# Performance work log

Hardware: AMD Instinct MI355X
Metric: run time of the kernel (lower is better)

Reference implementation:

```python
import jax, jax.numpy as jnp
import numpy as np

TOKENS_B, TOKENS_S, N_IN, N_OUT = 8, 2048, 4096, 4096
N8, N4 = 2048, 2048  # channels per format


def setup_inputs() -> dict:
    key = jax.random.key(0)
    k = jax.random.split(key, 7)
    x = jax.random.normal(k[0], (TOKENS_B, TOKENS_S, N_IN), dtype=jnp.float32)
    # int8-format group: values in [-128, 127], per-output-channel scale
    q8 = jax.random.randint(k[1], (N8, N_IN), -128, 128, dtype=jnp.int32)
    s8 = jax.random.uniform(k[2], (N8, 1), dtype=jnp.float32) * 0.01 + 1e-4
    # int4-format group: values in [-8, 7], per-output-channel scale
    q4 = jax.random.randint(k[3], (N4, N_IN), -8, 8, dtype=jnp.int32)
    s4 = jax.random.uniform(k[4], (N4, 1), dtype=jnp.float32) * 0.1 + 1e-4
    # inverse permutation restoring original channel order from [fmt8 | fmt4] concat
    inv_perm = jax.random.permutation(k[5], N_OUT).astype(jnp.int32)
    bias = jax.random.normal(k[6], (N_OUT,), dtype=jnp.float32) * 0.01
    return {"x": x, "q8": q8, "s8": s8, "q4": q4, "s4": s4,
            "inv_perm": inv_perm, "bias": bias}


def reference(x, q8, s8, q4, s4, inv_perm, bias):
    # Per-format dequantize: w = q * scale (per-output-channel scale)
    w8 = q8.astype(jnp.float32) * s8  # [N8, N_IN]
    w4 = q4.astype(jnp.float32) * s4  # [N4, N_IN]
    # Grouped GEMMs, one per format
    y8 = jnp.einsum('bsi,oi->bso', x, w8)  # [B, S, N8]
    y4 = jnp.einsum('bsi,oi->bso', x, w4)  # [B, S, N4]
    # Concat along output channels, then restore original channel order
    y = jnp.concatenate([y8, y4], axis=-1)  # [B, S, N_OUT]
    out = y[..., inv_perm] + bias
    return out
```

## Files before the change

kernel.cpp:

```cpp
#include <hip/hip_runtime.h>


#define M_TOK 16384
#define N_O   4096
#define K_IN  4096
#define N8F   2048
#define NT    (K_IN / 64)

typedef __attribute__((ext_vector_type(4))) int i32x4;

__device__ __forceinline__ void gl_lds16(const void* g, void* l) {
  __builtin_amdgcn_global_load_lds(
      (const __attribute__((address_space(1))) unsigned int*)g,
      (__attribute__((address_space(3))) unsigned int*)l, 16, 0, 0);
}

__device__ __forceinline__ int clampq(float f) {
  int q = (int)rintf(f);
  return q > 127 ? 127 : (q < -127 ? -127 : q);
}

__global__ void prep_kernel(const float* __restrict__ x,
                            const int4* __restrict__ q8, const float* __restrict__ s8,
                            const int4* __restrict__ q4, const float* __restrict__ s4,
                            const int* __restrict__ inv,
                            char* __restrict__ Wq, float* __restrict__ scale,
                            float* __restrict__ sx, char* __restrict__ xq) {
  __shared__ float red[4];
  const int t = threadIdx.x;
  if (blockIdx.x < N_O) {
    const int j = blockIdx.x;
    const int c = inv[j];
    const int4* src; float s;
    if (c < N8F) { src = q8 + (size_t)c * (K_IN / 4);         s = s8[c]; }
    else         { src = q4 + (size_t)(c - N8F) * (K_IN / 4); s = s4[c - N8F]; }
    if (t == 0) scale[j] = s;
    unsigned dw[4];
#pragma unroll
    for (int i = 0; i < 4; ++i) {
      int4 v = src[t * 4 + i];
      dw[i] = (v.x & 255) | ((v.y & 255) << 8) | ((v.z & 255) << 16)
            | ((unsigned)(v.w & 255) << 24);
    }
    *(uint4*)(Wq + (size_t)j * K_IN + t * 16) = make_uint4(dw[0], dw[1], dw[2], dw[3]);
  } else {
    const int T = blockIdx.x - N_O;
    const float4* xr = (const float4*)(x + (size_t)T * K_IN);
    float4 v[4];
    float m = 0.f;
#pragma unroll
    for (int i = 0; i < 4; ++i) {
      v[i] = xr[t * 4 + i];
      m = fmaxf(m, fmaxf(fmaxf(fabsf(v[i].x), fabsf(v[i].y)),
                         fmaxf(fabsf(v[i].z), fabsf(v[i].w))));
    }
#pragma unroll
    for (int o = 32; o; o >>= 1) m = fmaxf(m, __shfl_xor(m, o));
    if ((t & 63) == 0) red[t >> 6] = m;
    __syncthreads();
    m = fmaxf(fmaxf(red[0], red[1]), fmaxf(red[2], red[3]));
    const float rq = m > 0.f ? 127.f / m : 0.f;
    if (t == 0) sx[T] = m * (1.f / 127.f);
    unsigned dw[4];
#pragma unroll
    for (int i = 0; i < 4; ++i) {
      int a0 = clampq(v[i].x * rq), a1 = clampq(v[i].y * rq);
      int a2 = clampq(v[i].z * rq), a3 = clampq(v[i].w * rq);
      dw[i] = (a0 & 255) | ((a1 & 255) << 8) | ((a2 & 255) << 16)
            | ((unsigned)(a3 & 255) << 24);
    }
    *(uint4*)(xq + (size_t)T * K_IN + t * 16) = make_uint4(dw[0], dw[1], dw[2], dw[3]);
  }
}

__global__ __launch_bounds__(512, 4)
void gemm_i8(const char* __restrict__ xq, const char* __restrict__ Wq,
             const float* __restrict__ sx, const float* __restrict__ scale,
             const float* __restrict__ bias, float* __restrict__ out) {
  __shared__ __align__(16) char sm[49152];
  const int t = threadIdx.x;
  const int w = t >> 6, l = t & 63;
  const int wr = w >> 1, wc = w & 1;
  const int wg = blockIdx.x;
  const int xcd = wg & 7, idx = wg >> 3;
  const int bm = (xcd << 3) | (idx >> 5);
  const int bn = idx & 31;
  const int row0 = bm * 256, col0 = bn * 128;

  const int srow = l >> 2;
  const int schunk = (((l & 3) - ((l >> 3) & 3)) & 3) * 16;
  const char* aGw = xq + (size_t)(row0 + w * 32 + srow) * K_IN + schunk;
  const char* bGw = Wq + (size_t)(col0 + w * 16 + srow) * K_IN + schunk;

  auto stage = [&](int buf, int kt) {
    const int o = kt << 6;
    char* aD = sm + buf * 24576 + w * 2048;
    char* bD = sm + buf * 24576 + 16384 + w * 1024;
    gl_lds16(aGw + o, aD);
    gl_lds16(aGw + 16 * K_IN + o, aD + 1024);
    gl_lds16(bGw + o, bD);
  };

  const int rfoff = (l & 15) * 64 + ((((l >> 4) & 3) + (((l & 15) >> 1) & 3)) & 3) * 16;
  const char* rA0 = sm + rfoff;
  const char* rB0 = sm + 16384 + rfoff;

  i32x4 acc[4][4];
#pragma unroll
  for (int m = 0; m < 4; ++m)
#pragma unroll
    for (int n = 0; n < 4; ++n) acc[m][n] = (i32x4){0, 0, 0, 0};

  stage(0, 0);
  __syncthreads();

  for (int kt2 = 0; kt2 < NT; kt2 += 2) {
#pragma unroll
    for (int half = 0; half < 2; ++half) {
      const int kt = kt2 + half;
      const int cur = half;
      if (kt + 1 < NT) stage(cur ^ 1, kt + 1);

      const char* rA = rA0 + cur * 24576 + wr * 4096;
      const char* rB = rB0 + cur * 24576 + wc * 4096;
      i32x4 a[4], b[4];
#pragma unroll
      for (int n = 0; n < 4; ++n) b[n] = *(const i32x4*)(rB + n * 1024);
#pragma unroll
      for (int m = 0; m < 4; ++m) a[m] = *(const i32x4*)(rA + m * 1024);
#pragma unroll
      for (int m = 0; m < 4; ++m)
#pragma unroll
        for (int n = 0; n < 4; ++n)
          acc[m][n] = __builtin_amdgcn_mfma_i32_16x16x64_i8(a[m], b[n],
                                                            acc[m][n], 0, 0, 0);
      __syncthreads();
    }
  }

  const int orow0 = row0 + wr * 64 + ((l >> 4) << 2);
  const int ocol0 = col0 + wc * 64 + (l & 15);
#pragma unroll
  for (int n = 0; n < 4; ++n) {
    const int col = ocol0 + n * 16;
    const float sc = scale[col];
    const float bi = bias[col];
#pragma unroll
    for (int m = 0; m < 4; ++m) {
      const int r = orow0 + m * 16;
      const float4 sxv = *(const float4*)(sx + r);
      out[(size_t)(r + 0) * N_O + col] = (float)acc[m][n][0] * (sxv.x * sc) + bi;
      out[(size_t)(r + 1) * N_O + col] = (float)acc[m][n][1] * (sxv.y * sc) + bi;
      out[(size_t)(r + 2) * N_O + col] = (float)acc[m][n][2] * (sxv.z * sc) + bi;
      out[(size_t)(r + 3) * N_O + col] = (float)acc[m][n][3] * (sxv.w * sc) + bi;
    }
  }
}

extern "C" void kernel_launch(void* const* d_in, const int* in_sizes, int n_in,
                              void* d_out, int out_size, void* d_ws, size_t ws_size,
                              hipStream_t stream) {
  const float* x    = (const float*)d_in[0];
  const int*   q8   = (const int*)d_in[1];
  const float* s8   = (const float*)d_in[2];
  const int*   q4   = (const int*)d_in[3];
  const float* s4   = (const float*)d_in[4];
  const int*   inv  = (const int*)d_in[5];
  const float* bias = (const float*)d_in[6];
  float* out = (float*)d_out;

  char* ws = (char*)d_ws;
  char*  Wq    = ws;
  float* scale = (float*)(ws + (size_t)N_O * K_IN);
  float* sx    = (float*)(ws + (size_t)N_O * K_IN + 65536);
  char*  xq    = ws + (size_t)N_O * K_IN + 65536 + 65536;

  prep_kernel<<<N_O + M_TOK, 256, 0, stream>>>(x, (const int4*)q8, s8,
                                               (const int4*)q4, s4, inv,
                                               Wq, scale, sx, xq);
  gemm_i8<<<(M_TOK / 256) * (N_O / 128), 512, 0, stream>>>(xq, Wq, sx, scale,
                                                           bias, out);
}
```

Baseline: 428.6 us.

## Restructure int8 GEMM into 256x256 tiles with ping-pong wave groups

Each block's tile grows from 256x128 to 256x256, and the K step doubles to 128, with 128KB of LDS. The eight waves split into two groups of four that alternate between LDS reads and MFMA bursts, separated by explicit barriers and s_setprio. The intent is to raise arithmetic intensity and to overlap LDS traffic and global-to-LDS staging with matrix-core work. In exchange, occupancy drops to 2 blocks per CU, accumulator register pressure rises, the barrier schedule becomes intricate, and the XCD-aware block remapping is gone.

```diff
diff --git a/kernel.cpp b/kernel.cpp
--- a/kernel.cpp
+++ b/kernel.cpp
@@ -5,7 +5,7 @@
 #define N_O   4096
 #define K_IN  4096
 #define N8F   2048
-#define NT    (K_IN / 64)
+#define NT    (K_IN / 128)
 
 typedef __attribute__((ext_vector_type(4))) int i32x4;
 
@@ -73,80 +73,141 @@
   }
 }
 
-__global__ __launch_bounds__(512, 4)
+
+#define BAR  __builtin_amdgcn_s_barrier()
+#define SB0  __builtin_amdgcn_sched_barrier(0)
+#define LG0  asm volatile("s_waitcnt lgkmcnt(0)" ::: "memory")
+#define VM0  asm volatile("s_waitcnt vmcnt(0)" ::: "memory")
+
+#define RD_B(rB)                                                     \
+  _Pragma("unroll") for (int n_ = 0; n_ < 4; ++n_) {                 \
+    bfr[n_][0] = *(const i32x4*)((rB) + n_ * 2048 + cb0);            \
+    bfr[n_][1] = *(const i32x4*)((rB) + n_ * 2048 + (cb0 ^ 64));     \
+  }
+
+#define RD_A(rA, MB, DST)                                            \
+  _Pragma("unroll") for (int m_ = 0; m_ < 2; ++m_) {                 \
+    DST[m_][0] = *(const i32x4*)((rA) + ((MB) + m_) * 2048 + cb0);   \
+    DST[m_][1] = *(const i32x4*)((rA) + ((MB) + m_) * 2048 + (cb0 ^ 64)); \
+  }
+
+#define MFCL(MB, AF)                                                 \
+  __builtin_amdgcn_s_setprio(1);                                     \
+  _Pragma("unroll") for (int m_ = 0; m_ < 2; ++m_)                   \
+  _Pragma("unroll") for (int n_ = 0; n_ < 4; ++n_)                   \
+  _Pragma("unroll") for (int kk_ = 0; kk_ < 2; ++kk_)                \
+    acc[(MB) + m_][n_] = __builtin_amdgcn_mfma_i32_16x16x64_i8(      \
+        AF[m_][kk_], bfr[n_][kk_], acc[(MB) + m_][n_], 0, 0, 0);     \
+  __builtin_amdgcn_s_setprio(0);
+
+#define STAG_TILE(CUR, KT)                                           \
+  {                                                                  \
+    const char* rA = rAb + (CUR) * 16384;                            \
+    const char* rB = rBb + (CUR) * 32768;                            \
+                                                            \
+    if (isG0) { RD_B(rB); RD_A(rA, 0, afr); }                        \
+    else {                                                           \
+      if ((KT) > 0) { LG0; SB0; MFCL(6, afr2); }                     \
+      VM0; SB0;                                                      \
+    }                                                                \
+    BAR;                                                             \
+                                                            \
+    if (isG0) { LG0; SB0; MFCL(0, afr); }                            \
+    else { RD_B(rB); RD_A(rA, 0, afr); }                             \
+    BAR;                                                             \
+                                                            \
+    if (isG0) { RD_A(rA, 2, afr); }                                  \
+    else { LG0; SB0; MFCL(0, afr); }                                 \
+    BAR;                                                             \
+                                                            \
+    if (isG0) { if ((KT) + 2 < NT) stB((CUR), (KT) + 2);             \
+                LG0; SB0; MFCL(2, afr); }                            \
+    else { RD_A(rA, 2, afr); }                                       \
+    BAR;                                                             \
+                                                            \
+    if (isG0) { RD_A(rA, 4, afr); RD_A(rA, 6, afr2); }               \
+    else { if ((KT) + 2 < NT) stB((CUR), (KT) + 2);                  \
+           LG0; SB0; MFCL(2, afr); }                                 \
+    BAR;                                                             \
+                                                            \
+    if (isG0) { LG0; SB0; MFCL(4, afr); }                            \
+    else { RD_A(rA, 4, afr); RD_A(rA, 6, afr2); }                    \
+    BAR;                                                             \
+                                                            \
+    if (isG0) { if ((KT) + 1 < NT) stA((CUR) ^ 1, (KT) + 1); }       \
+    else { LG0; SB0; MFCL(4, afr); }                                 \
+    BAR;                                                             \
+                                                            \
+    if (isG0) { MFCL(6, afr2); VM0; SB0; }                           \
+    else { if ((KT) + 1 < NT) stA((CUR) ^ 1, (KT) + 1); }            \
+    BAR;                                                             \
+  }
+
+__global__ __launch_bounds__(512, 2)
 void gemm_i8(const char* __restrict__ xq, const char* __restrict__ Wq,
              const float* __restrict__ sx, const float* __restrict__ scale,
              const float* __restrict__ bias, float* __restrict__ out) {
-  __shared__ __align__(16) char sm[49152];
+  __shared__ __align__(16) char sm[131072];
   const int t = threadIdx.x;
   const int w = t >> 6, l = t & 63;
-  const int wr = w >> 1, wc = w & 1;
-  const int wg = blockIdx.x;
-  const int xcd = wg & 7, idx = wg >> 3;
-  const int bm = (xcd << 3) | (idx >> 5);
-  const int bn = idx & 31;
-  const int row0 = bm * 256, col0 = bn * 128;
-
-  const int srow = l >> 2;
-  const int schunk = (((l & 3) - ((l >> 3) & 3)) & 3) * 16;
-  const char* aGw = xq + (size_t)(row0 + w * 32 + srow) * K_IN + schunk;
-  const char* bGw = Wq + (size_t)(col0 + w * 16 + srow) * K_IN + schunk;
-
-  auto stage = [&](int buf, int kt) {
-    const int o = kt << 6;
-    char* aD = sm + buf * 24576 + w * 2048;
-    char* bD = sm + buf * 24576 + 16384 + w * 1024;
-    gl_lds16(aGw + o, aD);
-    gl_lds16(aGw + 16 * K_IN + o, aD + 1024);
-    gl_lds16(bGw + o, bD);
+  const int grp = w >> 2;
+  const int wq = w & 3;
+  const bool isG0 = (grp == 0);
+  const int bm = blockIdx.x >> 4, bn = blockIdx.x & 15;
+  const int row0 = bm * 256, col0 = bn * 256;
+
+  const int srow = l >> 3;
+  const int schunk = ((l & 7) ^ srow) * 16;
+  const char* aGs = xq + (size_t)(row0 + grp * 128 + wq * 32 + srow) * K_IN + schunk;
+  const char* bGs = Wq + (size_t)(col0 + grp * 128 + wq * 32 + srow) * K_IN + schunk;
+  char* aDb = sm + grp * 32768 + wq * 4096;
+  char* bDb = sm + 65536 + grp * 16384 + wq * 4096;
+
+  auto stA = [&](int buf, int kt) {
+#pragma unroll
+    for (int i = 0; i < 4; ++i)
+      gl_lds16(aGs + (size_t)(8 * i) * K_IN + ((size_t)kt << 7),
+               aDb + buf * 16384 + i * 1024);
   };
-
-  const int rfoff = (l & 15) * 64 + ((((l >> 4) & 3) + (((l & 15) >> 1) & 3)) & 3) * 16;
-  const char* rA0 = sm + rfoff;
-  const char* rB0 = sm + 16384 + rfoff;
-
-  i32x4 acc[4][4];
-#pragma unroll
-  for (int m = 0; m < 4; ++m)
+  auto stB = [&](int buf, int kt) {
+#pragma unroll
+    for (int i = 0; i < 4; ++i)
+      gl_lds16(bGs + (size_t)(8 * i) * K_IN + ((size_t)kt << 7),
+               bDb + buf * 32768 + i * 1024);
+  };
+
+  const int lrow128 = (l & 15) * 128;
+  const int cb0 = (((l >> 4) << 4) ^ ((l & 7) << 4));
+  const char* rAb = sm + grp * 32768 + lrow128;
+  const char* rBb = sm + 65536 + wq * 8192 + lrow128;
+
+  i32x4 acc[8][4];
+#pragma unroll
+  for (int m = 0; m < 8; ++m)
 #pragma unroll
     for (int n = 0; n < 4; ++n) acc[m][n] = (i32x4){0, 0, 0, 0};
 
-  stage(0, 0);
-  __syncthreads();
-
-  for (int kt2 = 0; kt2 < NT; kt2 += 2) {
-#pragma unroll
-    for (int half = 0; half < 2; ++half) {
-      const int kt = kt2 + half;
-      const int cur = half;
-      if (kt + 1 < NT) stage(cur ^ 1, kt + 1);
-
-      const char* rA = rA0 + cur * 24576 + wr * 4096;
-      const char* rB = rB0 + cur * 24576 + wc * 4096;
-      i32x4 a[4], b[4];
-#pragma unroll
-      for (int n = 0; n < 4; ++n) b[n] = *(const i32x4*)(rB + n * 1024);
-#pragma unroll
-      for (int m = 0; m < 4; ++m) a[m] = *(const i32x4*)(rA + m * 1024);
-#pragma unroll
-      for (int m = 0; m < 4; ++m)
-#pragma unroll
-        for (int n = 0; n < 4; ++n)
-          acc[m][n] = __builtin_amdgcn_mfma_i32_16x16x64_i8(a[m], b[n],
-                                                            acc[m][n], 0, 0, 0);
-      __syncthreads();
-    }
-  }
-
-  const int orow0 = row0 + wr * 64 + ((l >> 4) << 2);
-  const int ocol0 = col0 + wc * 64 + (l & 15);
+  stA(0, 0); stB(0, 0); stB(1, 1);
+  VM0;
+  BAR;
+
+  i32x4 bfr[4][2], afr[2][2], afr2[2][2];
+
+  for (int kt = 0; kt < NT; kt += 2) {
+    STAG_TILE(0, kt);
+    STAG_TILE(1, kt + 1);
+  }
+  if (!isG0) { LG0; SB0; MFCL(6, afr2); }
+
+  const int orow0 = row0 + grp * 128 + ((l >> 4) << 2);
+  const int ocol0 = col0 + wq * 64 + (l & 15);
 #pragma unroll
   for (int n = 0; n < 4; ++n) {
     const int col = ocol0 + n * 16;
     const float sc = scale[col];
     const float bi = bias[col];
 #pragma unroll
-    for (int m = 0; m < 4; ++m) {
+    for (int m = 0; m < 8; ++m) {
       const int r = orow0 + m * 16;
       const float4 sxv = *(const float4*)(sx + r);
       out[(size_t)(r + 0) * N_O + col] = (float)acc[m][n][0] * (sxv.x * sc) + bi;
@@ -178,6 +239,6 @@
   prep_kernel<<<N_O + M_TOK, 256, 0, stream>>>(x, (const int4*)q8, s8,
                                                (const int4*)q4, s4, inv,
                                                Wq, scale, sx, xq);
-  gemm_i8<<<(M_TOK / 256) * (N_O / 128), 512, 0, stream>>>(xq, Wq, sx, scale,
+  gemm_i8<<<(M_TOK / 256) * (N_O / 256), 512, 0, stream>>>(xq, Wq, sx, scale,
                                                            bias, out);
 }
```

After: 414.2 us. 3.3% less time.
